# Kernel optimization log

Measured on AMD Instinct MI355X. Metric: run time of the kernel, lower is better.

Reference implementation:

```python
import jax, jax.numpy as jnp
import numpy as np

HEADS, DHEAD = 4, 64            # TransformerConv heads / out_channels
MAX_EDGE_DIST = 1.0

def _ln(x, g, b):
    m = jnp.mean(x, -1, keepdims=True)
    v = jnp.mean((x - m) ** 2, -1, keepdims=True)
    return (x - m) * jax.lax.rsqrt(v + 1e-5) * g + b


def _embed_conv(node_feat, entity_type, adjv, mask, emb, W1, b1, g1, be1, Wh, bh, gh, beh):
    # aggr='add' message passing over dense masked adjacency. mask[b,s,t]: edge s->t.
    B, N, _ = mask.shape
    src = jnp.concatenate([node_feat, emb[entity_type]], -1)          # [B,N,F+E]
    msg = jnp.concatenate(
        [jnp.broadcast_to(src[:, :, None, :], (B, N, N, src.shape[-1])),
         adjv[..., None]], -1)                                        # [B,Ns,Nt,F+E+1]
    h = _ln(jax.nn.relu(msg @ W1 + b1), g1, be1)                      # lin1
    h = _ln(jax.nn.relu(h @ Wh + bh), gh, beh)                        # lin2[0]
    return jnp.einsum('bst,bsth->bth', mask, h)                       # sum over sources


def _tconv(x, adjv, mask, Wq, bq, Wk, bk, Wv, bv, We, Ws, bs):
    # PyG TransformerConv (beta=False, dropout=0, root_weight=True, concat=True).
    B, N, _ = x.shape
    q = (x @ Wq + bq).reshape(B, N, HEADS, DHEAD)
    k = (x @ Wk + bk).reshape(B, N, HEADS, DHEAD)
    v = (x @ Wv + bv).reshape(B, N, HEADS, DHEAD)
    we = We.reshape(HEADS, DHEAD)                                     # edge_dim=1, no bias
    scale = 1.0 / jnp.sqrt(jnp.asarray(DHEAD, x.dtype))
    # score[b,h,s,t] = q_t . (k_s + adjv[s,t]*we) * scale
    qk = jnp.einsum('bshd,bthd->bhst', k, q)
    qe = jnp.einsum('bthd,hd->bht', q, we)
    logits = (qk + adjv[:, None, :, :] * qe[:, :, None, :]) * scale
    mh = mask[:, None, :, :]                                          # [B,1,Ns,Nt]
    masked = jnp.where(mh > 0, logits, -1e30)
    mmax = jnp.max(masked, axis=2, keepdims=True)
    w = jnp.exp(masked - mmax) * mh
    den = jnp.sum(w, axis=2, keepdims=True)
    alpha = w / jnp.maximum(den, 1e-16)                               # softmax over sources per target
    out = jnp.einsum('bhst,bshd->bthd', alpha, v)
    out = out + jnp.einsum('bhst,bst->bth', alpha, adjv)[..., None] * we
    out = out.reshape(B, N, HEADS * DHEAD)
    return out + x @ Ws + bs                                          # skip (root) connection


def _forward(node_feat, entity_type, adj, agent_id, emb, W1, b1, g1, be1, Wh, bh, gh, beh,
             Wq1, bq1, Wk1, bk1, Wv1, bv1, We1, Ws1, bs1,
             Wq2, bq2, Wk2, bk2, Wv2, bv2, We2, Ws2, bs2):
    mask = ((adj > 0) & (adj < MAX_EDGE_DIST)).astype(adj.dtype)
    adjv = adj * mask
    x = _embed_conv(node_feat, entity_type, adjv, mask, emb, W1, b1, g1, be1, Wh, bh, gh, beh)
    x = jax.nn.relu(_tconv(x, adjv, mask, Wq1, bq1, Wk1, bk1, Wv1, bv1, We1, Ws1, bs1))
    x = jax.nn.relu(_tconv(x, adjv, mask, Wq2, bq2, Wk2, bk2, Wv2, bv2, We2, Ws2, bs2))
    return x[jnp.arange(x.shape[0]), agent_id]                        # gather agent node feats


def setup_inputs() -> dict:
    key = jax.random.key(0)
    ks = jax.random.split(key, 24)
    B, N, F, E, H = 32, 128, 9, 8, 128
    HD = HEADS * DHEAD
    s = 0.05
    p = lambda k, shape: (jax.random.normal(k, shape, jnp.float32) * s)
    inp = {
        'node_feat': jax.random.normal(ks[0], (B, N, F), jnp.float32),
        'entity_type': jax.random.randint(ks[1], (B, N), 0, 8),
        'adj': jax.random.uniform(ks[2], (B, N, N), jnp.float32, 0.0, 2.0),
        'agent_id': jax.random.randint(ks[3], (B,), 0, N),
        'emb': p(ks[4], (8, E)),
        'W1': p(ks[5], (F + E + 1, H)), 'b1': jnp.zeros(H), 'g1': jnp.ones(H), 'be1': jnp.zeros(H),
        'Wh': p(ks[6], (H, H)), 'bh': jnp.zeros(H), 'gh': jnp.ones(H), 'beh': jnp.zeros(H),
        'Wq1': p(ks[7], (H, HD)), 'bq1': jnp.zeros(HD),
        'Wk1': p(ks[8], (H, HD)), 'bk1': jnp.zeros(HD),
        'Wv1': p(ks[9], (H, HD)), 'bv1': jnp.zeros(HD),
        'We1': p(ks[10], (1, HD)),
        'Ws1': p(ks[11], (H, HD)), 'bs1': jnp.zeros(HD),
        'Wq2': p(ks[12], (HD, HD)), 'bq2': jnp.zeros(HD),
        'Wk2': p(ks[13], (HD, HD)), 'bk2': jnp.zeros(HD),
        'Wv2': p(ks[14], (HD, HD)), 'bv2': jnp.zeros(HD),
        'We2': p(ks[15], (1, HD)),
        'Ws2': p(ks[16], (HD, HD)), 'bs2': jnp.zeros(HD),
    }
    return inp


def reference(node_feat, entity_type, adj, agent_id, emb, W1, b1, g1, be1, Wh, bh, gh, beh,
              Wq1, bq1, Wk1, bk1, Wv1, bv1, We1, Ws1, bs1,
              Wq2, bq2, Wk2, bk2, Wv2, bv2, We2, Ws2, bs2):
    return _forward(node_feat, entity_type, adj, agent_id, emb, W1, b1, g1, be1, Wh, bh, gh, beh,
                    Wq1, bq1, Wk1, bk1, Wv1, bv1, We1, Ws1, bs1,
                    Wq2, bq2, Wk2, bk2, Wv2, bv2, We2, Ws2, bs2)
```

## Files before the change

kernel.cpp:

```cpp
#include <hip/hip_runtime.h>
#include <hip/hip_bf16.h>

typedef __hip_bfloat16 bf16;
typedef unsigned short ushort_t;
typedef unsigned char uchar_t;
typedef unsigned int uint_t;
typedef __attribute__((ext_vector_type(8))) short short8;
typedef __attribute__((ext_vector_type(4))) float fx4;
typedef __attribute__((ext_vector_type(4))) unsigned int uintx4;

#define BB 32
#define NN 128
#define FF 9
#define EE 8
#define HH 128
#define HD 256
#define NHEAD 4
#define DHEAD 64

__device__ __forceinline__ float us2f(ushort_t u) {
    return __uint_as_float(((unsigned int)u) << 16);
}
__device__ __forceinline__ ushort_t f2us_tr(float f) {
    return (ushort_t)(__float_as_uint(f) >> 16);
}
__device__ __forceinline__ short8 pack4(uint_t w0, uint_t w1, uint_t w2, uint_t w3) {
    uintx4 u = (uintx4){w0, w1, w2, w3};
    return __builtin_bit_cast(short8, u);
}
__device__ __forceinline__ void pair_split(float a, float c, uint_t& hw, uint_t& lw) {
    uint_t ua = __float_as_uint(a), uc = __float_as_uint(c);
    uint_t ka = ua & 0xffff0000u, kc = uc & 0xffff0000u;
    float la = a - __uint_as_float(ka);
    float lc = c - __uint_as_float(kc);
    hw = (ua >> 16) | kc;
    lw = (__float_as_uint(la) >> 16) | (__float_as_uint(lc) & 0xffff0000u);
}
__device__ __forceinline__ uint_t pair_hi(float a, float c) {
    return (__float_as_uint(a) >> 16) | (__float_as_uint(c) & 0xffff0000u);
}

__global__ void TransformerConvNet_85315230367963_kernel() {}

__global__ void k_sent(float* out, float val) {
    out[blockIdx.x * 256 + threadIdx.x] = val;
}

__global__ void __launch_bounds__(256) k_prep_all(
    const float* adj, float* adjvT, uchar_t* sl_s, float* sl_av, int* cnts,
    const float* nf, const int* et, const float* emb, const float* W1,
    const float* b1, float* base, float* x0,
    const float* Wh, const float* g1, const float* be1, const float* bh,
    ushort_t* BhiG, ushort_t* BloG, float* W1s, float* cbv,
    const float* Wq1, const float* Wk1, const float* Wv1, const float* Ws1,
    ushort_t* WhA, ushort_t* WlA,
    const float* Wq2, const float* Wk2, const float* Wv2, const float* Ws2,
    ushort_t* WhB, ushort_t* WlB)
{
    int blk = blockIdx.x;
    int tid = threadIdx.x;

    if (blk < 256) {
        int b = blk >> 3, sl = blk & 7;
        int wv = tid >> 6, lane = tid & 63;
#pragma unroll
        for (int j = 0; j < 8; j++) {
            int u = wv * 8 + j;
            int t = sl * 16 + (u >> 1);
            int sh = u & 1;
            int s = sh * 64 + lane;
            float a = adj[(b * NN + s) * NN + t];
            float av = (a > 0.f && a < 1.0f) ? a : 0.f;
            adjvT[(b * NN + t) * NN + s] = av;
            unsigned long long mask = __ballot(av != 0.f);
            int key = (b * NN + t) * 2 + sh;
            if (av != 0.f) {
                int pos = __popcll(mask & ((1ull << lane) - 1ull));
                sl_s[key * 64 + pos] = (uchar_t)s;
                sl_av[key * 64 + pos] = av;
            }
            if (lane == 0) {
                cnts[key] = (int)__popcll(mask);
                if (mask == 0ull) { sl_s[key * 64] = 0; sl_av[key * 64] = 0.f; }
            }
        }
    } else if (blk < 1280) {
        int bblk = blk - 256;
        int c = tid & 127;
#pragma unroll
        for (int rr = 0; rr < 2; rr++) {
            int bs = bblk * 4 + rr * 2 + (tid >> 7);
            int ty = et[bs];
            float acc = b1[c];
            for (int f = 0; f < FF; f++)
                acc += nf[bs * FF + f] * W1[f * HH + c];
            for (int e2 = 0; e2 < EE; e2++)
                acc += emb[ty * EE + e2] * W1[(FF + e2) * HH + c];
            base[bs * HH + c] = acc;
        }
    } else if (blk < 1536) {
        int zblk = blk - 1280;
        float4* p = (float4*)x0 + zblk * 512 + tid * 2;
        p[0] = (float4){0.f, 0.f, 0.f, 0.f};
        p[1] = (float4){0.f, 0.f, 0.f, 0.f};
    } else if (blk < 1568) {
        int n = (blk - 1536) * 4 + (tid >> 6);
        int t = tid & 63;
        int sw = 8 * (n & 15);
        float s1 = 0.f, s2 = 0.f;
#pragma unroll
        for (int kk = 0; kk < 2; kk++) {
            int k = t + kk * 64;
            float w = Wh[k * HH + n];
            float wp = g1[k] * w;
            ushort_t hb = f2us_tr(wp);
            float lo = wp - us2f(hb);
            BhiG[n * HH + (k ^ sw)] = hb;
            BloG[n * HH + (k ^ sw)] = f2us_tr(lo);
            s1 += wp;
            s2 += be1[k] * w;
        }
        for (int m = 1; m < 64; m <<= 1) {
            s1 += __shfl_xor(s1, m);
            s2 += __shfl_xor(s2, m);
        }
        if (t == 0) { W1s[n] = s1; cbv[n] = s2 + bh[n]; }
    } else if (blk < 1824) {
        int key = (blk - 1568) * 4 + (tid >> 6);
        int lane = tid & 63;
        int mat = key >> 8, n = key & 255;
        const float* W = (mat == 0) ? Wq1 : (mat == 1) ? Wk1 : (mat == 2) ? Wv1 : Ws1;
        ushort_t* hi = WhA + mat * 256 * HH;
        ushort_t* lo = WlA + mat * 256 * HH;
        int sw = 8 * (n & 15);
        for (int k = lane; k < HH; k += 64) {
            float w = W[k * HD + n];
            ushort_t hb = f2us_tr(w);
            float l = w - us2f(hb);
            hi[n * HH + (k ^ sw)] = hb;
            lo[n * HH + (k ^ sw)] = f2us_tr(l);
        }
    } else {
        int key = (blk - 1824) * 4 + (tid >> 6);
        int lane = tid & 63;
        int mat = key >> 8, n = key & 255;
        const float* W = (mat == 0) ? Wq2 : (mat == 1) ? Wk2 : (mat == 2) ? Wv2 : Ws2;
        ushort_t* hi = WhB + mat * 256 * HD;
        ushort_t* lo = WlB + mat * 256 * HD;
        int sw = 8 * (n & 15);
        for (int k = lane; k < HD; k += 64) {
            float w = W[k * HD + n];
            ushort_t hb = f2us_tr(w);
            float l = w - us2f(hb);
            hi[n * HD + (k ^ sw)] = hb;
            lo[n * HD + (k ^ sw)] = f2us_tr(l);
        }
    }
}

__global__ void __launch_bounds__(256) k_econv_mfma(
    const uchar_t* sl_s, const float* sl_av, const int* cnts,
    const float* base, const float* W1,
    const ushort_t* BhiG, const ushort_t* BloG,
    const float* W1sg, const float* cbv,
    const float* ghp, const float* behp, float* x0)
{
    __shared__ __align__(16) ushort_t PhiPlo[2 * HH * HH];
    __shared__ int tmap16[16];
    ushort_t* Phi = PhiPlo;
    ushort_t* Plo = PhiPlo + HH * HH;

    int blk = blockIdx.x;
    int b  = blk >> 4;
    int tt = (blk >> 1) & 7;
    int sh = blk & 1;
    if (b >= BB / 2) tt = 7 - tt;
    int t0 = tt * 16;
    int tid = threadIdx.x;
    int wv  = tid >> 6;
    int lane = tid & 63;
    int nl = lane & 15;
    int quad = lane >> 4;

    int* itmp = (int*)PhiPlo;
    if (tid < 128) itmp[tid] = cnts[((b << 7) + tid) * 2 + sh];
    __syncthreads();
    if (tid < 128) {
        int ci = itmp[tid];
        int rank = 0;
        for (int j = 0; j < 128; j++) {
            int cj = itmp[j];
            rank += (cj > ci) || (cj == ci && j < tid);
        }
        itmp[128 + rank] = tid;
    }
    __syncthreads();
    if (tid < 16) tmap16[tid] = itmp[128 + t0 + tid];
    __syncthreads();
    int myt = tmap16[nl];

    {
        const uint4* srcH = (const uint4*)BhiG;
        const uint4* srcL = (const uint4*)BloG;
        uint4* dstH = (uint4*)Phi;
        uint4* dstL = (uint4*)Plo;
        for (int i = tid; i < HH * HH / 8; i += 256) {
            dstH[i] = srcH[i];
            dstL[i] = srcL[i];
        }
    }

    float w17v[4][8];
#pragma unroll
    for (int st = 0; st < 4; st++) {
        const float* p = W1 + 17 * HH + quad * 8 + 32 * st;
        float4 a = *(const float4*)p;
        float4 bq = *(const float4*)(p + 4);
        w17v[st][0] = a.x;  w17v[st][1] = a.y;  w17v[st][2] = a.z;  w17v[st][3] = a.w;
        w17v[st][4] = bq.x; w17v[st][5] = bq.y; w17v[st][6] = bq.z; w17v[st][7] = bq.w;
    }

    int key = ((b << 7) + myt) * 2 + sh;
    int cnt = cnts[key];
    int q = (cnt + 3) >> 2;
    int mq = q;
#pragma unroll
    for (int m = 1; m < 16; m <<= 1) mq = max(mq, __shfl_xor(mq, m));
    const uchar_t* lst_s = sl_s + key * 64;
    const float*   lst_a = sl_av + key * 64;
    int i0 = wv * q;

    fx4 acc1[8];
#pragma unroll
    for (int tile = 0; tile < 8; tile++) acc1[tile] = (fx4){0.f, 0.f, 0.f, 0.f};
    float c0 = 0.f;
    float c1 = 0.f;

    __syncthreads();

    for (int i = 0; i < mq; i++) {
        int idx = i0 + i;
        bool val = (i < q) && (idx < cnt);
        int ridx = (idx < cnt) ? idx : (cnt > 0 ? cnt - 1 : 0);
        int s = lst_s[ridx];
        float avv = val ? lst_a[ridx] : 0.f;
        const float* brow = base + (b * NN + s) * HH;

        short8 Hhi[4], Hlo[4];
        float sm = 0.f, s2 = 0.f;
#pragma unroll
        for (int st = 0; st < 4; st++) {
            const float* p = brow + quad * 8 + 32 * st;
            float4 b0 = *(const float4*)p;
            float4 b1q = *(const float4*)(p + 4);
            float h[8] = {b0.x, b0.y, b0.z, b0.w, b1q.x, b1q.y, b1q.z, b1q.w};
            uint_t hw[4], lw[4];
#pragma unroll
            for (int pr = 0; pr < 4; pr++) {
                float a = fmaxf(fmaf(avv, w17v[st][2 * pr], h[2 * pr]), 0.f);
                float c = fmaxf(fmaf(avv, w17v[st][2 * pr + 1], h[2 * pr + 1]), 0.f);
                sm += a; sm += c;
                s2 = fmaf(a, a, s2);
                s2 = fmaf(c, c, s2);
                pair_split(a, c, hw[pr], lw[pr]);
            }
            Hhi[st] = pack4(hw[0], hw[1], hw[2], hw[3]);
            Hlo[st] = pack4(lw[0], lw[1], lw[2], lw[3]);
        }
        sm += __shfl_xor(sm, 16); sm += __shfl_xor(sm, 32);
        s2 += __shfl_xor(s2, 16); s2 += __shfl_xor(s2, 32);
        float m1 = sm * (1.f / 128.f);
        float r1 = rsqrtf(s2 * (1.f / 128.f) - m1 * m1 + 1e-5f);
        float nm = -m1 * r1;

        fx4 G[8];
#pragma unroll
        for (int tile = 0; tile < 8; tile++) G[tile] = (fx4){0.f, 0.f, 0.f, 0.f};
#pragma unroll
        for (int st = 0; st < 4; st++) {
            int koff = quad * 8 + 32 * st;
#pragma unroll
            for (int tile = 0; tile < 8; tile++) {
                int off = (tile * 16 + nl) * HH + (koff ^ (nl * 8));
                short8 ph = *(const short8*)(&Phi[off]);
                short8 pl = *(const short8*)(&Plo[off]);
                G[tile] = __builtin_amdgcn_mfma_f32_16x16x32_bf16(ph, Hhi[st], G[tile], 0, 0, 0);
                G[tile] = __builtin_amdgcn_mfma_f32_16x16x32_bf16(pl, Hhi[st], G[tile], 0, 0, 0);
                G[tile] = __builtin_amdgcn_mfma_f32_16x16x32_bf16(ph, Hlo[st], G[tile], 0, 0, 0);
            }
        }

        float sm2 = 0.f, ss2 = 0.f;
#pragma unroll
        for (int tile = 0; tile < 8; tile++) {
            float4 w4 = *(const float4*)(W1sg + tile * 16 + quad * 4);
            float4 c4 = *(const float4*)(cbv + tile * 16 + quad * 4);
            float wa[4] = {w4.x, w4.y, w4.z, w4.w};
            float ca[4] = {c4.x, c4.y, c4.z, c4.w};
#pragma unroll
            for (int r = 0; r < 4; r++) {
                float pre = fmaf(r1, G[tile][r], fmaf(nm, wa[r], ca[r]));
                float h2 = fmaxf(pre, 0.f);
                G[tile][r] = h2;
                sm2 += h2;
                ss2 = fmaf(h2, h2, ss2);
            }
        }
        sm2 += __shfl_xor(sm2, 16); sm2 += __shfl_xor(sm2, 32);
        ss2 += __shfl_xor(ss2, 16); ss2 += __shfl_xor(ss2, 32);
        float mean2 = sm2 * (1.f / 128.f);
        float r2 = rsqrtf(ss2 * (1.f / 128.f) - mean2 * mean2 + 1e-5f);
        float msk = val ? 1.f : 0.f;
        float mr2 = msk * r2;

#pragma unroll
        for (int tile = 0; tile < 8; tile++)
#pragma unroll
            for (int r = 0; r < 4; r++)
                acc1[tile][r] = fmaf(mr2, G[tile][r], acc1[tile][r]);
        c0 += msk;
        c1 = fmaf(mr2, mean2, c1);
    }

    __syncthreads();
    float* slab = (float*)PhiPlo;
#pragma unroll
    for (int tile = 0; tile < 8; tile++) {
        float4 g4 = *(const float4*)(ghp + tile * 16 + quad * 4);
        float4 be4 = *(const float4*)(behp + tile * 16 + quad * 4);
        float gv[4] = {g4.x, g4.y, g4.z, g4.w};
        float bv[4] = {be4.x, be4.y, be4.z, be4.w};
#pragma unroll
        for (int r = 0; r < 4; r++) {
            float xv = fmaf(gv[r], acc1[tile][r] - c1, bv[r] * c0);
            slab[(wv * 16 + nl) * 132 + tile * 16 + quad * 4 + r] = xv;
        }
    }
    __syncthreads();
    for (int e = tid; e < 16 * HH; e += 256) {
        int t = e >> 7, n = e & 127;
        float vsum = slab[t * 132 + n] + slab[(16 + t) * 132 + n]
                   + slab[(32 + t) * 132 + n] + slab[(48 + t) * 132 + n];
        atomicAdd(&x0[(b * NN + tmap16[t]) * HH + n], vsum);
    }
}

template <int IN>
__global__ void __launch_bounds__(256) k_qkvs_mfma(
    const float* x, const ushort_t* Whi, const ushort_t* Wlo,
    const float* b0, const float* b1, const float* b2, const float* b3,
    float* q, float* skipo,
    ushort_t* khi, ushort_t* klo, ushort_t* vThi, ushort_t* vTlo,
    const int* agentp)
{
    const int ST = IN / 32;
    int blk = blockIdx.x;
    int m0 = (blk >> 3) * 64;
    int nsl = blk & 7;
    int tid = threadIdx.x;
    int wv = tid >> 6;
    int lane = tid & 63;
    int nl = lane & 15;
    int quad = lane >> 4;
    int row = m0 + wv * 16 + nl;

    short8 Ahi[ST], Alo[ST];
    const float* xrow = x + (long)row * IN;
#pragma unroll
    for (int st = 0; st < ST; st++) {
        const float* p = xrow + quad * 8 + 32 * st;
        float4 a4 = *(const float4*)p;
        float4 b4 = *(const float4*)(p + 4);
        float h[8] = {a4.x, a4.y, a4.z, a4.w, b4.x, b4.y, b4.z, b4.w};
        uint_t hw[4], lw[4];
#pragma unroll
        for (int pr = 0; pr < 4; pr++)
            pair_split(h[2 * pr], h[2 * pr + 1], hw[pr], lw[pr]);
        Ahi[st] = pack4(hw[0], hw[1], hw[2], hw[3]);
        Alo[st] = pack4(lw[0], lw[1], lw[2], lw[3]);
    }

    const float* bs_[4] = {b0, b1, b2, b3};
    int rw0 = m0 + wv * 16;
    bool agset = (agentp != nullptr);
    int agrow = agset ? agentp[rw0 >> 7] : -1;
    bool havea = agset && ((agrow >> 4) == ((rw0 & 127) >> 4));

#pragma unroll
    for (int mat = 0; mat < 4; mat++) {
        if ((mat == 0 || mat == 3) && agset && !havea) continue;
        const ushort_t* Bh = Whi + (mat * 256 + nsl * 32) * IN;
        const ushort_t* Bl = Wlo + (mat * 256 + nsl * 32) * IN;
        fx4 G[2];
#pragma unroll
        for (int tile = 0; tile < 2; tile++) {
            float bc = bs_[mat][nsl * 32 + tile * 16 + nl];
            G[tile] = (fx4){bc, bc, bc, bc};
        }
#pragma unroll
        for (int st = 0; st < ST; st++) {
            int koff = quad * 8 + 32 * st;
#pragma unroll
            for (int tile = 0; tile < 2; tile++) {
                int off = (tile * 16 + nl) * IN + (koff ^ (nl * 8));
                short8 bh8 = *(const short8*)(Bh + off);
                short8 bl8 = *(const short8*)(Bl + off);
                G[tile] = __builtin_amdgcn_mfma_f32_16x16x32_bf16(Ahi[st], bh8, G[tile], 0, 0, 0);
                G[tile] = __builtin_amdgcn_mfma_f32_16x16x32_bf16(Alo[st], bh8, G[tile], 0, 0, 0);
                G[tile] = __builtin_amdgcn_mfma_f32_16x16x32_bf16(Ahi[st], bl8, G[tile], 0, 0, 0);
            }
        }
        int row0 = m0 + wv * 16 + quad * 4;
        if (mat == 0 || mat == 3) {
            float* om = (mat == 0) ? q : skipo;
#pragma unroll
            for (int tile = 0; tile < 2; tile++)
#pragma unroll
                for (int r = 0; r < 4; r++)
                    om[(row0 + r) * HD + nsl * 32 + tile * 16 + nl] = G[tile][r];
        } else if (mat == 1) {
#pragma unroll
            for (int tile = 0; tile < 2; tile++) {
                int col = nsl * 32 + tile * 16 + nl;
#pragma unroll
                for (int r = 0; r < 4; r++) {
                    float gv = G[tile][r];
                    ushort_t hb = f2us_tr(gv);
                    khi[(row0 + r) * HD + col] = hb;
                    klo[(row0 + r) * HD + col] = f2us_tr(gv - us2f(hb));
                }
            }
        } else {
            int bb = row0 >> 7;
            int s0 = row0 & 127;
#pragma unroll
            for (int tile = 0; tile < 2; tile++) {
                int col = nsl * 32 + tile * 16 + nl;
                int dg = bb * 256 + col;
                ushort4 h4, l4;
                float g0 = G[tile][0], g1 = G[tile][1], g2 = G[tile][2], g3 = G[tile][3];
                ushort_t h0 = f2us_tr(g0), h1 = f2us_tr(g1), h2 = f2us_tr(g2), h3 = f2us_tr(g3);
                h4.x = h0; h4.y = h1; h4.z = h2; h4.w = h3;
                l4.x = f2us_tr(g0 - us2f(h0));
                l4.y = f2us_tr(g1 - us2f(h1));
                l4.z = f2us_tr(g2 - us2f(h2));
                l4.w = f2us_tr(g3 - us2f(h3));
                *(ushort4*)&vThi[dg * NN + s0] = h4;
                *(ushort4*)&vTlo[dg * NN + s0] = l4;
            }
        }
    }
}

__global__ void __launch_bounds__(128) k_attn_mfma(
    const float* qb, const ushort_t* khi, const ushort_t* klo,
    const ushort_t* vThi, const ushort_t* vTlo,
    const float* adjvT, const float* We, const float* skip, float* xout,
    const int* agentp, float* outp)
{
    __shared__ float aL[16][132];
    __shared__ float qeL[16];
    __shared__ float mxL[2][16];
    __shared__ float dnL[2][16];
    __shared__ float ebL[2][16];

    int blk = blockIdx.x;
    int b, h, tt;
    if (agentp == nullptr) {
        b = blk >> 5; h = (blk >> 3) & 3; tt = blk & 7;
    } else {
        b = blk >> 2; h = blk & 3; tt = agentp[b] >> 4;
    }
    int t0 = tt * 16;
    int tid = threadIdx.x;
    int w   = tid >> 6;
    int lane = tid & 63;
    int nl = lane & 15;
    int quad = lane >> 4;

    short8 Qhi[2], Qlo[2];
    float qe = 0.f;
#pragma unroll
    for (int ks = 0; ks < 2; ks++) {
        const float* p = qb + (b * NN + t0 + nl) * HD + h * DHEAD + quad * 8 + 32 * ks;
        const float* wp = We + h * DHEAD + quad * 8 + 32 * ks;
        float4 a0 = *(const float4*)p;
        float4 a1 = *(const float4*)(p + 4);
        float4 w0 = *(const float4*)wp;
        float4 w1 = *(const float4*)(wp + 4);
        float hv[8] = {a0.x, a0.y, a0.z, a0.w, a1.x, a1.y, a1.z, a1.w};
        float wv8[8] = {w0.x, w0.y, w0.z, w0.w, w1.x, w1.y, w1.z, w1.w};
        uint_t hw[4], lw[4];
#pragma unroll
        for (int pr = 0; pr < 4; pr++) {
            float a = hv[2 * pr], c = hv[2 * pr + 1];
            qe = fmaf(a, wv8[2 * pr], qe);
            qe = fmaf(c, wv8[2 * pr + 1], qe);
            pair_split(a, c, hw[pr], lw[pr]);
        }
        Qhi[ks] = pack4(hw[0], hw[1], hw[2], hw[3]);
        Qlo[ks] = pack4(lw[0], lw[1], lw[2], lw[3]);
    }
    qe += __shfl_xor(qe, 16);
    qe += __shfl_xor(qe, 32);
    if (w == 0 && lane < 16) qeL[lane] = qe;
    __syncthreads();
    float qe_r[4];
#pragma unroll
    for (int r = 0; r < 4; r++) qe_r[r] = qeL[quad * 4 + r];
    float we_d[2];
#pragma unroll
    for (int nt2 = 0; nt2 < 2; nt2++) we_d[nt2] = We[h * DHEAD + (w * 2 + nt2) * 16 + nl];

    fx4 S[4];
#pragma unroll
    for (int st = 0; st < 4; st++) S[st] = (fx4){0.f, 0.f, 0.f, 0.f};
#pragma unroll
    for (int ks = 0; ks < 2; ks++) {
#pragma unroll
        for (int st = 0; st < 4; st++) {
            long off = (long)(b * NN + (w * 4 + st) * 16 + nl) * HD + h * DHEAD + quad * 8 + 32 * ks;
            short8 bh8 = *(const short8*)(khi + off);
            short8 bl8 = *(const short8*)(klo + off);
            S[st] = __builtin_amdgcn_mfma_f32_16x16x32_bf16(Qhi[ks], bh8, S[st], 0, 0, 0);
            S[st] = __builtin_amdgcn_mfma_f32_16x16x32_bf16(Qlo[ks], bh8, S[st], 0, 0, 0);
            S[st] = __builtin_amdgcn_mfma_f32_16x16x32_bf16(Qhi[ks], bl8, S[st], 0, 0, 0);
        }
    }

    float av[4][4];
#pragma unroll
    for (int st = 0; st < 4; st++)
#pragma unroll
        for (int r = 0; r < 4; r++)
            av[st][r] = adjvT[(b * NN + t0 + quad * 4 + r) * NN + (w * 4 + st) * 16 + nl];
#pragma unroll
    for (int st = 0; st < 4; st++)
#pragma unroll
        for (int r = 0; r < 4; r++) {
            float a = av[st][r];
            S[st][r] = (a != 0.f) ? (S[st][r] + a * qe_r[r]) * 0.125f : -1e30f;
        }

    float mxp[4];
#pragma unroll
    for (int r = 0; r < 4; r++) {
        float m = S[0][r];
#pragma unroll
        for (int st = 1; st < 4; st++) m = fmaxf(m, S[st][r]);
#pragma unroll
        for (int mm = 1; mm < 16; mm <<= 1) m = fmaxf(m, __shfl_xor(m, mm));
        mxp[r] = m;
    }
    if (nl == 0) {
#pragma unroll
        for (int r = 0; r < 4; r++) mxL[w][quad * 4 + r] = mxp[r];
    }
    __syncthreads();
    float mx[4];
#pragma unroll
    for (int r = 0; r < 4; r++)
        mx[r] = fmaxf(mxL[0][quad * 4 + r], mxL[1][quad * 4 + r]);

    float dnp[4] = {0.f, 0.f, 0.f, 0.f}, ebp[4] = {0.f, 0.f, 0.f, 0.f};
#pragma unroll
    for (int st = 0; st < 4; st++)
#pragma unroll
        for (int r = 0; r < 4; r++) {
            float e = (av[st][r] != 0.f) ? __expf(S[st][r] - mx[r]) : 0.f;
            S[st][r] = e;
            dnp[r] += e;
            ebp[r] = fmaf(e, av[st][r], ebp[r]);
        }
#pragma unroll
    for (int r = 0; r < 4; r++) {
#pragma unroll
        for (int mm = 1; mm < 16; mm <<= 1) {
            dnp[r] += __shfl_xor(dnp[r], mm);
            ebp[r] += __shfl_xor(ebp[r], mm);
        }
    }
    if (nl == 0) {
#pragma unroll
        for (int r = 0; r < 4; r++) {
            dnL[w][quad * 4 + r] = dnp[r];
            ebL[w][quad * 4 + r] = ebp[r];
        }
    }
    __syncthreads();
    float rden[4], beta[4];
#pragma unroll
    for (int r = 0; r < 4; r++) {
        int row = quad * 4 + r;
        float d = dnL[0][row] + dnL[1][row];
        rden[r] = 1.f / fmaxf(d, 1e-16f);
        beta[r] = (ebL[0][row] + ebL[1][row]) * rden[r];
    }

#pragma unroll
    for (int st = 0; st < 4; st++)
#pragma unroll
        for (int r = 0; r < 4; r++)
            aL[quad * 4 + r][(w * 4 + st) * 16 + nl] = S[st][r] * rden[r];
    __syncthreads();

    short8 Ah[4];
#pragma unroll
    for (int ks = 0; ks < 4; ks++) {
        const float* p = &aL[nl][quad * 8 + 32 * ks];
        float4 a0 = *(const float4*)p;
        float4 a1 = *(const float4*)(p + 4);
        float hv[8] = {a0.x, a0.y, a0.z, a0.w, a1.x, a1.y, a1.z, a1.w};
        uint_t ww[4];
#pragma unroll
        for (int pr = 0; pr < 4; pr++) ww[pr] = pair_hi(hv[2 * pr], hv[2 * pr + 1]);
        Ah[ks] = pack4(ww[0], ww[1], ww[2], ww[3]);
    }

    fx4 G[2];
#pragma unroll
    for (int nt2 = 0; nt2 < 2; nt2++) {
        fx4 g;
#pragma unroll
        for (int r = 0; r < 4; r++) g[r] = beta[r] * we_d[nt2];
        G[nt2] = g;
    }
#pragma unroll
    for (int ks = 0; ks < 4; ks++) {
#pragma unroll
        for (int nt2 = 0; nt2 < 2; nt2++) {
            long dg = (long)(b * 256 + h * DHEAD + (w * 2 + nt2) * 16 + nl);
            const short8 vh = *(const short8*)(vThi + dg * NN + quad * 8 + 32 * ks);
            const short8 vl = *(const short8*)(vTlo + dg * NN + quad * 8 + 32 * ks);
            G[nt2] = __builtin_amdgcn_mfma_f32_16x16x32_bf16(Ah[ks], vh, G[nt2], 0, 0, 0);
            G[nt2] = __builtin_amdgcn_mfma_f32_16x16x32_bf16(Ah[ks], vl, G[nt2], 0, 0, 0);
        }
    }

    if (agentp == nullptr) {
#pragma unroll
        for (int nt2 = 0; nt2 < 2; nt2++)
#pragma unroll
            for (int r = 0; r < 4; r++) {
                int gi = (b * NN + t0 + quad * 4 + r) * HD + h * DHEAD + (w * 2 + nt2) * 16 + nl;
                xout[gi] = fmaxf(G[nt2][r] + skip[gi], 0.f);
            }
    } else {
        int ag = agentp[b];
#pragma unroll
        for (int nt2 = 0; nt2 < 2; nt2++)
#pragma unroll
            for (int r = 0; r < 4; r++) {
                int t = t0 + quad * 4 + r;
                if (t == ag) {
                    int d = h * DHEAD + (w * 2 + nt2) * 16 + nl;
                    int gi = (b * NN + t) * HD + d;
                    outp[b * HD + d] = fmaxf(G[nt2][r] + skip[gi], 0.f);
                }
            }
    }
}

extern "C" void kernel_launch(void* const* d_in, const int* in_sizes, int n_in,
                              void* d_out, int out_size, void* d_ws, size_t ws_size,
                              hipStream_t stream) {
    float* out = (float*)d_out;
    (void)hipGetLastError();

    bool ok = (n_in == 31) && in_sizes[0] == BB * NN * FF && in_sizes[2] == BB * NN * NN
              && in_sizes[5] == (FF + EE + 1) * HH && in_sizes[13] == HH * HD
              && in_sizes[22] == HD * HD && out_size == BB * HD;
    if (!ok) { k_sent<<<32, 256, 0, stream>>>(out, -30000.f); return; }

    const size_t WS_NEED = (size_t)8912896 * 4;
    if (ws_size < WS_NEED) { k_sent<<<32, 256, 0, stream>>>(out, -20000.f); return; }

    const float* nf    = (const float*)d_in[0];
    const int*   et    = (const int*)d_in[1];
    const float* adj   = (const float*)d_in[2];
    const int*   agent = (const int*)d_in[3];
    const float* emb   = (const float*)d_in[4];
    const float* W1    = (const float*)d_in[5];
    const float* b1    = (const float*)d_in[6];
    const float* g1    = (const float*)d_in[7];
    const float* be1   = (const float*)d_in[8];
    const float* Wh    = (const float*)d_in[9];
    const float* bh    = (const float*)d_in[10];
    const float* gh    = (const float*)d_in[11];
    const float* beh   = (const float*)d_in[12];
    const float* Wq1   = (const float*)d_in[13];
    const float* bq1   = (const float*)d_in[14];
    const float* Wk1   = (const float*)d_in[15];
    const float* bk1   = (const float*)d_in[16];
    const float* Wv1   = (const float*)d_in[17];
    const float* bv1   = (const float*)d_in[18];
    const float* We1   = (const float*)d_in[19];
    const float* Ws1   = (const float*)d_in[20];
    const float* bs1   = (const float*)d_in[21];
    const float* Wq2   = (const float*)d_in[22];
    const float* bq2   = (const float*)d_in[23];
    const float* Wk2   = (const float*)d_in[24];
    const float* bk2   = (const float*)d_in[25];
    const float* Wv2   = (const float*)d_in[26];
    const float* bv2   = (const float*)d_in[27];
    const float* We2   = (const float*)d_in[28];
    const float* Ws2   = (const float*)d_in[29];
    const float* bs2   = (const float*)d_in[30];

    float* ws   = (float*)d_ws;
    float* slav = ws;
    float* base = ws + 524288;
    float* x0   = base + BB * NN * HH;
    float* q    = x0 + BB * NN * HH;
    float* kreg = q + BB * NN * HD;
    float* vreg = kreg + BB * NN * HD;
    float* skip = vreg + BB * NN * HD;
    float* areg = skip + BB * NN * HD;
    float* x1   = areg + BB * NN * HD;
    float* x2   = x1 + BB * NN * HD;

    ushort_t* BhiG = (ushort_t*)q;
    ushort_t* BloG = BhiG + HH * HH;
    float*    W1sW = q + 16384;
    float*    cbW  = q + 16512;
    int*      cnts = (int*)(q + 17024);

    ushort_t* khi  = (ushort_t*)kreg;
    ushort_t* klo  = khi + BB * NN * HD;
    ushort_t* vThi = (ushort_t*)vreg;
    ushort_t* vTlo = vThi + BB * NN * HD;

    ushort_t* WhA = (ushort_t*)areg;
    ushort_t* WlA = WhA + 4 * 256 * HH;
    ushort_t* WhB = WlA + 4 * 256 * HH;
    ushort_t* WlB = WhB + 4 * 256 * HD;
    float* adjvT  = areg + 393216;
    uchar_t* sl_s = (uchar_t*)(areg + 917504);

    int fail = 0;
    hipError_t e;
#define CHK(stage) do { e = hipGetLastError(); if (e != hipSuccess && fail == 0) fail = (stage); } while (0)

    k_prep_all<<<2080, 256, 0, stream>>>(
        adj, adjvT, sl_s, slav, cnts,
        nf, et, emb, W1, b1, base, x0,
        Wh, g1, be1, bh, BhiG, BloG, W1sW, cbW,
        Wq1, Wk1, Wv1, Ws1, WhA, WlA,
        Wq2, Wk2, Wv2, Ws2, WhB, WlB);                                               CHK(1);

    k_econv_mfma<<<512, 256, 0, stream>>>(sl_s, slav, cnts, base, W1,
                                          BhiG, BloG, W1sW, cbW, gh, beh, x0);       CHK(2);

    k_qkvs_mfma<HH><<<512, 256, 0, stream>>>(x0, WhA, WlA, bq1, bk1, bv1, bs1,
                                             q, skip, khi, klo, vThi, vTlo,
                                             nullptr);                               CHK(3);
    k_attn_mfma<<<1024, 128, 0, stream>>>(q, khi, klo, vThi, vTlo, adjvT, We1,
                                          skip, x1, nullptr, nullptr);               CHK(4);

    k_qkvs_mfma<HD><<<512, 256, 0, stream>>>(x1, WhB, WlB, bq2, bk2, bv2, bs2,
                                             q, skip, khi, klo, vThi, vTlo,
                                             agent);                                 CHK(5);
    k_attn_mfma<<<128, 128, 0, stream>>>(q, khi, klo, vThi, vTlo, adjvT, We2,
                                         skip, x2, agent, out);                      CHK(6);
#undef CHK

    if (fail != 0)
        k_sent<<<32, 256, 0, stream>>>(out, -(1000.f + 500.f * (float)fail));
}
```

Before: 249.9 us.

## Precompute per-batch target ranking in prep kernel and coalesce adjacency transpose via LDS

The per-target count ranking (an O(128^2) sort) used to be repeated in every econv block. It now runs once per batch inside the prep kernel and is stored as a global tmap. The adjacency pass changes from 256 blocks doing strided column reads to 32 blocks that stage 128x32 tiles in padded shared memory, so global reads are coalesced. In exchange, adjacency work is concentrated in far fewer blocks, which could lengthen the prep kernel's critical path, and econv drops two barriers.

```diff
diff --git a/kernel.cpp b/kernel.cpp
--- a/kernel.cpp
+++ b/kernel.cpp
@@ -48,6 +48,7 @@
 
 __global__ void __launch_bounds__(256) k_prep_all(
     const float* adj, float* adjvT, uchar_t* sl_s, float* sl_av, int* cnts,
+    int* tmapG,
     const float* nf, const int* et, const float* emb, const float* W1,
     const float* b1, float* base, float* x0,
     const float* Wh, const float* g1, const float* be1, const float* bh,
@@ -57,35 +58,62 @@
     const float* Wq2, const float* Wk2, const float* Wv2, const float* Ws2,
     ushort_t* WhB, ushort_t* WlB)
 {
+    __shared__ float tileF[128 * 33];
+    __shared__ int   cntL[256];
+
     int blk = blockIdx.x;
     int tid = threadIdx.x;
 
-    if (blk < 256) {
-        int b = blk >> 3, sl = blk & 7;
+    if (blk < 32) {
+        int b = blk;
         int wv = tid >> 6, lane = tid & 63;
-#pragma unroll
-        for (int j = 0; j < 8; j++) {
-            int u = wv * 8 + j;
-            int t = sl * 16 + (u >> 1);
-            int sh = u & 1;
-            int s = sh * 64 + lane;
-            float a = adj[(b * NN + s) * NN + t];
-            float av = (a > 0.f && a < 1.0f) ? a : 0.f;
-            adjvT[(b * NN + t) * NN + s] = av;
-            unsigned long long mask = __ballot(av != 0.f);
-            int key = (b * NN + t) * 2 + sh;
-            if (av != 0.f) {
-                int pos = __popcll(mask & ((1ull << lane) - 1ull));
-                sl_s[key * 64 + pos] = (uchar_t)s;
-                sl_av[key * 64 + pos] = av;
-            }
-            if (lane == 0) {
-                cnts[key] = (int)__popcll(mask);
-                if (mask == 0ull) { sl_s[key * 64] = 0; sl_av[key * 64] = 0.f; }
-            }
-        }
-    } else if (blk < 1280) {
-        int bblk = blk - 256;
+        for (int c = 0; c < 4; c++) {
+            int t0c = c * 32;
+#pragma unroll
+            for (int pass = 0; pass < 16; pass++) {
+                int s = pass * 8 + (tid >> 5);
+                int tq = tid & 31;
+                float a = adj[(b * NN + s) * NN + t0c + tq];
+                float av = (a > 0.f && a < 1.0f) ? a : 0.f;
+                tileF[s * 33 + tq] = av;
+            }
+            __syncthreads();
+#pragma unroll
+            for (int j = 0; j < 16; j++) {
+                int u = wv * 16 + j;
+                int tq = u >> 1, sh = u & 1;
+                int t = t0c + tq;
+                int s = sh * 64 + lane;
+                float av = tileF[s * 33 + tq];
+                adjvT[(b * NN + t) * NN + s] = av;
+                unsigned long long mask = __ballot(av != 0.f);
+                int key = (b * NN + t) * 2 + sh;
+                if (av != 0.f) {
+                    int pos = __popcll(mask & ((1ull << lane) - 1ull));
+                    sl_s[key * 64 + pos] = (uchar_t)s;
+                    sl_av[key * 64 + pos] = av;
+                }
+                if (lane == 0) {
+                    int cv = (int)__popcll(mask);
+                    cnts[key] = cv;
+                    cntL[t * 2 + sh] = cv;
+                    if (mask == 0ull) { sl_s[key * 64] = 0; sl_av[key * 64] = 0.f; }
+                }
+            }
+            __syncthreads();
+        }
+        {
+            int sh = tid >> 7, i = tid & 127;
+            int ci = cntL[i * 2 + sh];
+            int rank = 0;
+            for (int j = 0; j < 128; j++) {
+                int cj = cntL[j * 2 + sh];
+                rank += (cj > ci) || (cj == ci && j < i);
+            }
+            tmapG[b * 256 + sh * 128 + rank] = i;
+        }
+    } else if (blk < 1056) {
+        int bblk = blk - 32;
         int c = tid & 127;
 #pragma unroll
         for (int rr = 0; rr < 2; rr++) {
@@ -98,13 +126,13 @@
                 acc += emb[ty * EE + e2] * W1[(FF + e2) * HH + c];
             base[bs * HH + c] = acc;
         }
-    } else if (blk < 1536) {
-        int zblk = blk - 1280;
+    } else if (blk < 1312) {
+        int zblk = blk - 1056;
         float4* p = (float4*)x0 + zblk * 512 + tid * 2;
         p[0] = (float4){0.f, 0.f, 0.f, 0.f};
         p[1] = (float4){0.f, 0.f, 0.f, 0.f};
-    } else if (blk < 1568) {
-        int n = (blk - 1536) * 4 + (tid >> 6);
+    } else if (blk < 1344) {
+        int n = (blk - 1312) * 4 + (tid >> 6);
         int t = tid & 63;
         int sw = 8 * (n & 15);
         float s1 = 0.f, s2 = 0.f;
@@ -125,8 +153,8 @@
             s2 += __shfl_xor(s2, m);
         }
         if (t == 0) { W1s[n] = s1; cbv[n] = s2 + bh[n]; }
-    } else if (blk < 1824) {
-        int key = (blk - 1568) * 4 + (tid >> 6);
+    } else if (blk < 1600) {
+        int key = (blk - 1344) * 4 + (tid >> 6);
         int lane = tid & 63;
         int mat = key >> 8, n = key & 255;
         const float* W = (mat == 0) ? Wq1 : (mat == 1) ? Wk1 : (mat == 2) ? Wv1 : Ws1;
@@ -141,7 +169,7 @@
             lo[n * HH + (k ^ sw)] = f2us_tr(l);
         }
     } else {
-        int key = (blk - 1824) * 4 + (tid >> 6);
+        int key = (blk - 1600) * 4 + (tid >> 6);
         int lane = tid & 63;
         int mat = key >> 8, n = key & 255;
         const float* W = (mat == 0) ? Wq2 : (mat == 1) ? Wk2 : (mat == 2) ? Wv2 : Ws2;
@@ -159,7 +187,7 @@
 }
 
 __global__ void __launch_bounds__(256) k_econv_mfma(
-    const uchar_t* sl_s, const float* sl_av, const int* cnts,
+    const uchar_t* sl_s, const float* sl_av, const int* cnts, const int* tmapG,
     const float* base, const float* W1,
     const ushort_t* BhiG, const ushort_t* BloG,
     const float* W1sg, const float* cbv,
@@ -182,22 +210,7 @@
     int nl = lane & 15;
     int quad = lane >> 4;
 
-    int* itmp = (int*)PhiPlo;
-    if (tid < 128) itmp[tid] = cnts[((b << 7) + tid) * 2 + sh];
-    __syncthreads();
-    if (tid < 128) {
-        int ci = itmp[tid];
-        int rank = 0;
-        for (int j = 0; j < 128; j++) {
-            int cj = itmp[j];
-            rank += (cj > ci) || (cj == ci && j < tid);
-        }
-        itmp[128 + rank] = tid;
-    }
-    __syncthreads();
-    if (tid < 16) tmap16[tid] = itmp[128 + t0 + tid];
-    __syncthreads();
-    int myt = tmap16[nl];
+    if (tid < 16) tmap16[tid] = tmapG[b * 256 + sh * 128 + t0 + tid];
 
     {
         const uint4* srcH = (const uint4*)BhiG;
@@ -220,6 +233,9 @@
         w17v[st][4] = bq.x; w17v[st][5] = bq.y; w17v[st][6] = bq.z; w17v[st][7] = bq.w;
     }
 
+    __syncthreads();
+
+    int myt = tmap16[nl];
     int key = ((b << 7) + myt) * 2 + sh;
     int cnt = cnts[key];
     int q = (cnt + 3) >> 2;
@@ -235,8 +251,6 @@
     for (int tile = 0; tile < 8; tile++) acc1[tile] = (fx4){0.f, 0.f, 0.f, 0.f};
     float c0 = 0.f;
     float c1 = 0.f;
-
-    __syncthreads();
 
     for (int i = 0; i < mq; i++) {
         int idx = i0 + i;
@@ -724,6 +738,7 @@
     float*    W1sW = q + 16384;
     float*    cbW  = q + 16512;
     int*      cnts = (int*)(q + 17024);
+    int*      tmapG = (int*)(q + 25216);
 
     ushort_t* khi  = (ushort_t*)kreg;
     ushort_t* klo  = khi + BB * NN * HD;
@@ -741,14 +756,14 @@
     hipError_t e;
 #define CHK(stage) do { e = hipGetLastError(); if (e != hipSuccess && fail == 0) fail = (stage); } while (0)
 
-    k_prep_all<<<2080, 256, 0, stream>>>(
-        adj, adjvT, sl_s, slav, cnts,
+    k_prep_all<<<1856, 256, 0, stream>>>(
+        adj, adjvT, sl_s, slav, cnts, tmapG,
         nf, et, emb, W1, b1, base, x0,
         Wh, g1, be1, bh, BhiG, BloG, W1sW, cbW,
         Wq1, Wk1, Wv1, Ws1, WhA, WlA,
         Wq2, Wk2, Wv2, Ws2, WhB, WlB);                                               CHK(1);
 
-    k_econv_mfma<<<512, 256, 0, stream>>>(sl_s, slav, cnts, base, W1,
+    k_econv_mfma<<<512, 256, 0, stream>>>(sl_s, slav, cnts, tmapG, base, W1,
                                           BhiG, BloG, W1sW, cbW, gh, beh, x0);       CHK(2);
 
     k_qkvs_mfma<HH><<<512, 256, 0, stream>>>(x0, WhA, WlA, bq1, bk1, bv1, bs1,
```

Measured after the change: 253.5 us. No clear change (+1.4%).
